# Performance work log

Hardware: AMD Instinct MI355X
Metric: run time of the kernel (lower is better)

## Reference

```python
import jax, jax.numpy as jnp
import numpy as np

B, I, C, H, QP, VP = 2, 1024, 16, 12, 4, 8
W_C = (2.0 / (9.0 * QP)) ** 0.5
W_L = (1.0 / 3.0) ** 0.5


def setup_inputs() -> dict:
    key = jax.random.key(0)
    ks = jax.random.split(key, 14)
    rn = lambda k, shape, s=1.0: (jax.random.normal(k, shape, dtype=jnp.float32) * s)
    return {
        "s": rn(ks[0], (B, I, C)),
        "z": rn(ks[1], (B, I, I, C)),
        "R": rn(ks[2], (B, I, 3, 3)),
        "t": rn(ks[3], (B, I, 3)),
        "Wq": rn(ks[4], (C, C * H), C ** -0.5),
        "Wk": rn(ks[5], (C, C * H), C ** -0.5),
        "Wv": rn(ks[6], (C, C * H), C ** -0.5),
        "Wb": rn(ks[7], (C, H), C ** -0.5),
        "Wqp": rn(ks[8], (C, 3 * QP * H), C ** -0.5),
        "Wkp": rn(ks[9], (C, 3 * QP * H), C ** -0.5),
        "Wvp": rn(ks[10], (C, 3 * VP * H), C ** -0.5),
        "gamma": rn(ks[11], (H,), 0.5),
        "Wout": rn(ks[12], (H * (2 * C + 4 * VP), C), (H * (2 * C + 4 * VP)) ** -0.5),
        "bout": rn(ks[13], (C,), 0.02),
    }


def _apply_rigid(R, t, p):
    # p: (B, i, n, 3); rigid transform per residue: R @ p + t
    return jnp.einsum("bixy,bipy->bipx", R, p) + t[:, :, None, :]


def reference(s, z, R, t, Wq, Wk, Wv, Wb, Wqp, Wkp, Wvp, gamma, Wout, bout):
    b_, i_, c = s.shape
    h, qp, vp = gamma.shape[0], Wqp.shape[1] // (3 * gamma.shape[0]), Wvp.shape[1] // (3 * gamma.shape[0])

    q = (s @ Wq).reshape(b_, i_, h, c)
    k = (s @ Wk).reshape(b_, i_, h, c)
    v = (s @ Wv).reshape(b_, i_, h, c)

    q_pts = _apply_rigid(R, t, (s @ Wqp).reshape(b_, i_, h * qp, 3)).reshape(b_, i_, h, qp, 3)
    k_pts = _apply_rigid(R, t, (s @ Wkp).reshape(b_, i_, h * qp, 3)).reshape(b_, i_, h, qp, 3)
    v_pts = _apply_rigid(R, t, (s @ Wvp).reshape(b_, i_, h * vp, 3)).reshape(b_, i_, h, vp, 3)

    bias = jnp.einsum("bijc,ch->bhij", z, Wb)
    a = jnp.einsum("bihc,bjhc->bhij", q, k) * (c ** -0.5) + bias

    # squared point distances summed over points, expanded to avoid (B,i,j,h,P,3) tensor
    q2 = jnp.sum(q_pts ** 2, axis=(-1, -2))          # (B,i,h)
    k2 = jnp.sum(k_pts ** 2, axis=(-1, -2))          # (B,j,h)
    qk = jnp.einsum("bihpx,bjhpx->bhij", q_pts, k_pts)
    d2 = q2.transpose(0, 2, 1)[..., None] + k2.transpose(0, 2, 1)[:, :, None, :] - 2.0 * qk  # (B,h,i,j)

    head_w = jax.nn.softplus(gamma)                  # (h,)
    a = a + d2 * (head_w[None, :, None, None] * W_C * -0.5)
    a = a * W_L
    a = jax.nn.softmax(a, axis=-2)  # NOTE: original code softmaxes over dim=-2 (the i axis)

    # NOTE: original einsum indexes v by i (not j); replicated faithfully
    o = jnp.einsum("bhij,bihc->bihc", a, v).reshape(b_, i_, h * c)

    o_pts = jnp.einsum("bhij,bjhpx->bihpx", a, v_pts)  # (B,i,h,vp,3)
    o_pts_norm = jnp.sqrt(jnp.maximum(jnp.sum(o_pts ** 2, axis=-1), 1e-12)).reshape(b_, i_, h * vp)
    o_pts_flat = o_pts.reshape(b_, i_, h * vp * 3)

    o_pair = jnp.einsum("bhij,bijc->bihc", a, z).reshape(b_, i_, h * c)

    cat = jnp.concatenate([o, o_pair, o_pts_flat, o_pts_norm], axis=-1)
    return cat @ Wout + bout
```

## Files before the change

kernel.cpp:

```cpp
#include <hip/hip_runtime.h>
#include <hip/hip_bf16.h>
#include <math.h>

#define B_ 2
#define I_ 1024
#define C_ 16
#define H_ 12
#define ICH 8

__device__ __constant__ float kW_C = 0.23570226039551584f;
#define W_Lc 0.5773502691896258f
#define LOG2E 1.4426950408889634f

typedef _Float16 hf;
typedef hf hf2 __attribute__((ext_vector_type(2)));
typedef hf hf4v __attribute__((ext_vector_type(4)));
typedef hf hf8v __attribute__((ext_vector_type(8)));
typedef float f32x4 __attribute__((ext_vector_type(4)));
typedef unsigned int u32;

template <typename T, typename F>
__device__ inline T bc(F f) { return __builtin_bit_cast(T, f); }

__device__ inline float fdot2f(u32 a, u32 b, float c) {
#if __has_builtin(__builtin_amdgcn_fdot2)
  return __builtin_amdgcn_fdot2(bc<hf2>(a), bc<hf2>(b), c, false);
#else
  hf2 x = bc<hf2>(a), y = bc<hf2>(b);
  return c + (float)x[0] * (float)y[0] + (float)x[1] * (float)y[1];
#endif
}

__device__ inline u32 pkrtz(float lo, float hi) {
#if __has_builtin(__builtin_amdgcn_cvt_pkrtz)
  return bc<u32>(__builtin_amdgcn_cvt_pkrtz(lo, hi));
#else
  hf2 t; t[0] = (hf)lo; t[1] = (hf)hi; return bc<u32>(t);
#endif
}

__device__ inline u32 permlo(u32 hiw, u32 low) {
#if __has_builtin(__builtin_amdgcn_perm)
  return __builtin_amdgcn_perm(hiw, low, 0x05040100u);
#else
  return (low & 0xffffu) | (hiw << 16);
#endif
}
__device__ inline u32 permhi(u32 hiw, u32 low) {
#if __has_builtin(__builtin_amdgcn_perm)
  return __builtin_amdgcn_perm(hiw, low, 0x07060302u);
#else
  return (low >> 16) | (hiw & 0xffff0000u);
#endif
}

#define QF16_OFF 0
#define QF16_SZ (B_*I_*196)
#define KF16_OFF (QF16_OFF + QF16_SZ)
#define KF16_SZ QF16_SZ
#define VPF_OFF (KF16_OFF + KF16_SZ)
#define VPF_SZ (B_*I_*144)
#define VV_OFF (VPF_OFF + VPF_SZ)
#define VV_SZ (B_*I_*192)
#define SM_OFF (VV_OFF + VV_SZ)
#define SM_SZ (B_*12*1024*2)
#define PM_OFF (SM_OFF + SM_SZ)
#define PM_SZ (B_*64*ICH*192*2)
#define LT_OFF (PM_OFF + PM_SZ)
#define LT_SZ (B_*H_*512*1024)
#define ACC2_OFF (LT_OFF + LT_SZ)

__global__ __launch_bounds__(192) void kA(const float* __restrict__ s, const float* __restrict__ R,
                 const float* __restrict__ t, const float* __restrict__ Wq,
                 const float* __restrict__ Wk, const float* __restrict__ Wv,
                 const float* __restrict__ Wqp, const float* __restrict__ Wkp,
                 const float* __restrict__ Wvp, const float* __restrict__ gam,
                 float* __restrict__ ws) {
  int blk = blockIdx.x;
  int b = blk >> 10, i = blk & 1023;
  int tid = threadIdx.x;
  __shared__ float sl[16], rl[9], tl[3], part[96];
  if (tid < 16) sl[tid] = s[(b*I_ + i)*C_ + tid];
  else if (tid < 25) rl[tid-16] = R[(size_t)(b*I_+i)*9 + (tid-16)];
  else if (tid < 28) tl[tid-25] = t[(size_t)(b*I_+i)*3 + (tid-25)];
  __syncthreads();
  hf* QF  = (hf*)(ws + QF16_OFF) + (size_t)(b*I_+i)*392;
  hf* KF  = (hf*)(ws + KF16_OFF) + (size_t)(b*I_+i)*392;
  ushort* VPP = (ushort*)(ws + VPF_OFF);
  float* vv = ws + VV_OFF + (size_t)(b*I_+i)*192;
  {
    int hc = tid; int h = hc >> 4, c = hc & 15;
    float aq = 0.f, ak = 0.f, av = 0.f;
    #pragma unroll
    for (int ci = 0; ci < 16; ci++) {
      float sv = sl[ci];
      aq += sv * Wq[ci*192 + hc];
      ak += sv * Wk[ci*192 + hc];
      av += sv * Wv[ci*192 + hc];
    }
    const float s_qk = 0.25f * W_Lc * LOG2E;
    QF[h*32 + c] = (hf)(aq * s_qk);
    KF[h*32 + c] = (hf)ak;
    vv[hc] = av;
  }
  {
    float raw[3], px[3];
    if (tid < 96) {
      bool isq = tid < 48;
      int n = isq ? tid : tid - 48;
      const float* W = isq ? Wqp : Wkp;
      #pragma unroll
      for (int x = 0; x < 3; x++) {
        float a2 = 0.f;
        #pragma unroll
        for (int ci = 0; ci < 16; ci++) a2 += sl[ci] * W[ci*144 + n*3 + x];
        raw[x] = a2;
      }
      #pragma unroll
      for (int x = 0; x < 3; x++)
        px[x] = rl[x*3]*raw[0] + rl[x*3+1]*raw[1] + rl[x*3+2]*raw[2] + tl[x];
      int h = n >> 2, p = n & 3;
      part[tid] = px[0]*px[0] + px[1]*px[1] + px[2]*px[2];
      if (isq) {
        float g = gam[h];
        float sp = log1pf(expf(g));
        float coef2 = -0.5f * kW_C * sp * W_Lc * LOG2E;
        #pragma unroll
        for (int x = 0; x < 3; x++) QF[h*32 + 16 + p*3 + x] = (hf)(px[x] * (-2.0f * coef2));
      } else {
        #pragma unroll
        for (int x = 0; x < 3; x++) KF[h*32 + 16 + p*3 + x] = (hf)px[x];
      }
    } else {
      int n = tid - 96;
      #pragma unroll
      for (int x = 0; x < 3; x++) {
        float a2 = 0.f;
        #pragma unroll
        for (int ci = 0; ci < 16; ci++) a2 += sl[ci] * Wvp[ci*288 + n*3 + x];
        raw[x] = a2;
      }
      #pragma unroll
      for (int x = 0; x < 3; x++)
        px[x] = rl[x*3]*raw[0] + rl[x*3+1]*raw[1] + rl[x*3+2]*raw[2] + tl[x];
      int h = n >> 3, p = n & 7;
      size_t base = ((size_t)(b*512 + (i >> 1))*12 + h)*48 + (i & 1);
      #pragma unroll
      for (int x = 0; x < 3; x++) VPP[base + (p*3 + x)*2] = bc<ushort>((hf)px[x]);
    }
  }
  __syncthreads();
  if (tid < 24) {
    int h = tid % 12; bool isq = tid < 12;
    float g = gam[h];
    float sp = log1pf(expf(g));
    float coef2 = -0.5f * kW_C * sp * W_Lc * LOG2E;
    float s2 = 0.f;
    int base = isq ? h*4 : 48 + h*4;
    #pragma unroll
    for (int p = 0; p < 4; p++) s2 += part[base + p];
    if (isq) {
      QF[h*32 + 28] = (hf)(coef2 * s2);
      QF[h*32 + 29] = (hf)1.0f;
      QF[h*32 + 30] = (hf)0.0f;
      QF[h*32 + 31] = (hf)0.0f;
    } else {
      KF[h*32 + 28] = (hf)1.0f;
      KF[h*32 + 29] = (hf)(coef2 * s2);
      KF[h*32 + 30] = (hf)0.0f;
      KF[h*32 + 31] = (hf)0.0f;
    }
  }
}

__global__ __launch_bounds__(256,4) void kB(const float* __restrict__ z,
                 const float* __restrict__ Wb, float* __restrict__ ws) {
  int blk = blockIdx.x;
  int ic = blk & (ICH-1); int jt = (blk >> 3) & 63; int b = blk >> 9;
  int tid = threadIdx.x;
  int w = tid >> 6, lane = tid & 63;
  int ln15 = lane & 15, l16 = lane >> 4;
  int j0 = jt*16;
  __shared__ ushort qlds[16*392];
  __shared__ u32 lqk[12*16*18];
  __shared__ ushort lbias[16*208];
  __shared__ u32 llog[96*17];
  hf8v kf[3];
  #pragma unroll
  for (int q = 0; q < 3; q++) {
    int h = w*3 + q;
    const ushort* src = (const ushort*)(ws + KF16_OFF) + ((size_t)(b*I_ + j0 + ln15)*392 + h*32 + l16*8);
    kf[q] = *(const hf8v*)src;
  }
  hf4v wbf;
  #pragma unroll
  for (int e = 0; e < 4; e++) {
    int c = l16*4 + e;
    float v = (ln15 < 12) ? Wb[c*12 + ln15] * (W_Lc*LOG2E) : 0.f;
    wbf[e] = (hf)v;
  }
  u32* LTu_w = (u32*)(ws + LT_OFF);
  float m = -1e30f, S = 0.f;
  for (int t = 0; t < 8; ++t) {
    int i0 = ic*128 + t*16;
    __syncthreads();
    {
      const uint4* qsrc = (const uint4*)((const hf*)(ws + QF16_OFF) + (size_t)(b*I_+i0)*392);
      uint4* qdst = (uint4*)qlds;
      for (int idx = tid; idx < 784; idx += 256) qdst[idx] = qsrc[idx];
    }
    __syncthreads();
    #pragma unroll
    for (int q = 0; q < 3; q++) {
      int h = w*3 + q;
      hf8v a = *(const hf8v*)&qlds[ln15*392 + h*32 + l16*8];
      f32x4 c = {0.f, 0.f, 0.f, 0.f};
      c = __builtin_amdgcn_mfma_f32_16x16x32_f16(a, kf[q], c, 0, 0, 0);
      u32* dst = &lqk[(h*16 + ln15)*18 + l16*4];
      *(uint2*)dst     = make_uint2(bc<u32>(c[0]), bc<u32>(c[1]));
      *(uint2*)(dst+2) = make_uint2(bc<u32>(c[2]), bc<u32>(c[3]));
    }
    #pragma unroll
    for (int r = 0; r < 4; r++) {
      int ii = w*4 + r;
      float4 zv = *(const float4*)(z + ((size_t)(b*I_ + i0 + ii)*I_ + j0 + ln15)*16 + l16*4);
      uint2 ap = make_uint2(pkrtz(zv.x, zv.y), pkrtz(zv.z, zv.w));
      hf4v a = bc<hf4v>(ap);
      f32x4 cb = {0.f, 0.f, 0.f, 0.f};
      cb = __builtin_amdgcn_mfma_f32_16x16x16f16(a, wbf, cb, 0, 0, 0);
      if (ln15 < 12) {
        #pragma unroll
        for (int reg = 0; reg < 4; reg++) {
          int jj = l16*4 + reg;
          lbias[ii*208 + jj*13 + ln15] = bc<ushort>((hf)cb[reg]);
        }
      }
    }
    __syncthreads();
    if (tid < 192) {
      int h = tid >> 4, jl = tid & 15;
      const u32* qk = &lqk[(h*16 + jl)*18];
      float l[16];
      #pragma unroll
      for (int i = 0; i < 16; i++) l[i] = bc<float>(qk[i]);
      #pragma unroll
      for (int i = 0; i < 16; i++) l[i] += (float)bc<hf>(lbias[i*208 + jl*13 + h]);
      u32 lw[8];
      #pragma unroll
      for (int p = 0; p < 8; p++) lw[p] = pkrtz(l[2*p], l[2*p+1]);
      float lr[16];
      #pragma unroll
      for (int p = 0; p < 8; p++) { hf2 lh = bc<hf2>(lw[p]); lr[2*p] = (float)lh[0]; lr[2*p+1] = (float)lh[1]; }
      float m8[8];
      #pragma unroll
      for (int p = 0; p < 8; p++) m8[p] = fmaxf(lr[2*p], lr[2*p+1]);
      float mt = fmaxf(fmaxf(fmaxf(m8[0],m8[1]), fmaxf(m8[2],m8[3])),
                       fmaxf(fmaxf(m8[4],m8[5]), fmaxf(m8[6],m8[7])));
      float e[16];
      #pragma unroll
      for (int p = 0; p < 16; p++) e[p] = __builtin_amdgcn_exp2f(lr[p] - mt);
      float st = ((e[0]+e[1])+(e[2]+e[3])) + ((e[4]+e[5])+(e[6]+e[7]))
               + ((e[8]+e[9])+(e[10]+e[11])) + ((e[12]+e[13])+(e[14]+e[15]));
      float mn = fmaxf(m, mt);
      S = S * __builtin_amdgcn_exp2f(m - mn) + st * __builtin_amdgcn_exp2f(mt - mn);
      m = mn;
      #pragma unroll
      for (int p = 0; p < 8; p++) {
        u32 pw = (u32)__shfl_xor((int)lw[p], 1);
        u32 ex = (jl & 1) ? permhi(lw[p], pw) : permlo(pw, lw[p]);
        llog[(h*8 + (jl>>1))*17 + 2*p + (jl&1)] = ex;
      }
    }
    __syncthreads();
    if (tid < 192) {
      int row = tid >> 1, iseg = (tid & 1) << 3;
      const u32* lr2 = &llog[row*17 + iseg];
      u32 o0=lr2[0],o1=lr2[1],o2=lr2[2],o3=lr2[3],o4=lr2[4],o5=lr2[5],o6=lr2[6],o7=lr2[7];
      int hh = row >> 3, jpg2 = row & 7;
      u32* dst = LTu_w + ((size_t)(b*12+hh)*512 + jt*8 + jpg2)*1024 + i0 + iseg;
      *(uint4*)dst = make_uint4(o0,o1,o2,o3);
      *(uint4*)(dst+4) = make_uint4(o4,o5,o6,o7);
    }
  }
  if (tid < 192) {
    float2* pm = (float2*)(ws + PM_OFF);
    pm[((size_t)(b*64+jt)*ICH + ic)*192 + tid] = make_float2(m, S);
  }
}

__global__ __launch_bounds__(192) void kB2(float* __restrict__ ws) {
  int blk = blockIdx.x; int jt = blk & 63, b = blk >> 6;
  int tid = threadIdx.x; int h = tid >> 4, jl = tid & 15;
  const float2* pm = (const float2*)(ws + PM_OFF) + (size_t)(b*64+jt)*ICH*192 + tid;
  float m = -1e30f, S = 0.f;
  #pragma unroll
  for (int ic = 0; ic < ICH; ic++) {
    float2 p = pm[ic*192];
    float mn = fmaxf(m, p.x);
    S = S * __builtin_amdgcn_exp2f(m - mn) + p.y * __builtin_amdgcn_exp2f(p.x - mn);
    m = mn;
  }
  int j = jt*16 + jl;
  float* sm = ws + SM_OFF + ((size_t)((b*12+h)*1024) + j)*2;
  sm[0] = m;
  sm[1] = 1.0f / S;
}

__global__ __launch_bounds__(192,6) void kC(const float* __restrict__ z,
                 float* __restrict__ ws, int jsh) {
  int blk = blockIdx.x;
  int jch = 1 << jsh;
  int jc = blk & (jch-1); int it = (blk >> jsh) & 63; int b = blk >> (jsh+6);
  int tid = threadIdx.x; int h = tid >> 4, il = tid & 15;
  int i = it*16 + il;
  __shared__ u32 llds[96*18];
  __shared__ u32 zplds[16*132];
  float opts[24], opair[16], rsum = 0.f;
  #pragma unroll
  for (int n = 0; n < 24; n++) opts[n] = 0.f;
  #pragma unroll
  for (int c = 0; c < 16; c++) opair[c] = 0.f;
  const u32* LTu = (const u32*)(ws + LT_OFF);
  const float* SM = ws + SM_OFF + (size_t)((b*12+h)*1024)*2;
  const ushort* VPP = (const ushort*)(ws + VPF_OFF);
  int chunk = I_ >> jsh;
  int nt = chunk >> 4;
  int hh = tid >> 4, rr = tid & 15, sjp = rr >> 1, sq = rr & 1;
  for (int t = 0; t < nt; ++t) {
    int j0 = jc*chunk + t*16;
    int jpg0 = j0 >> 1;
    __syncthreads();
    {
      const u32* src = LTu + ((size_t)(b*12+hh)*512 + jpg0 + sjp)*1024 + it*16 + sq*8;
      uint4 a = *(const uint4*)src;
      uint4 c4 = *(const uint4*)(src + 4);
      u32* drow = llds + (hh*8 + sjp)*18 + sq*8;
      *(uint2*)(drow + 0) = make_uint2(a.x, a.y);
      *(uint2*)(drow + 2) = make_uint2(a.z, a.w);
      *(uint2*)(drow + 4) = make_uint2(c4.x, c4.y);
      *(uint2*)(drow + 6) = make_uint2(c4.z, c4.w);
    }
    for (int idx = tid; idx < 512; idx += 192) {
      int r = idx >> 5, jp = (idx >> 2) & 7, c4 = idx & 3;
      const float* zb = z + ((size_t)(b*I_ + it*16 + r)*I_ + j0 + 2*jp)*16 + c4*4;
      float4 a = *(const float4*)zb;
      float4 d = *(const float4*)(zb + 16);
      uint4 o = make_uint4(pkrtz(a.x, d.x), pkrtz(a.y, d.y), pkrtz(a.z, d.z), pkrtz(a.w, d.w));
      *(uint4*)&zplds[r*132 + jp*16 + c4*4] = o;
    }
    __syncthreads();
    #pragma unroll 1
    for (int jp = 0; jp < 8; ++jp) {
      u32 lp = llds[(h*8 + jp)*18 + il];
      float4 st = *(const float4*)(SM + (size_t)(j0 + 2*jp)*2);
      const uint4* vp4 = (const uint4*)(VPP + ((size_t)(b*512 + jpg0 + jp)*12 + h)*48);
      uint4 va = vp4[0], vb = vp4[1], vc = vp4[2];
      uint4 vd = vp4[3], ve = vp4[4], vf = vp4[5];
      hf2 lh = bc<hf2>(lp);
      float w0 = __builtin_amdgcn_exp2f((float)lh[0] - st.x) * st.y;
      float w1 = __builtin_amdgcn_exp2f((float)lh[1] - st.z) * st.w;
      rsum += w0 + w1;
      u32 w2 = pkrtz(w0, w1);
      const u32* zr = &zplds[il*132 + jp*16];
      uint4 p0 = *(const uint4*)(zr + 0), p1 = *(const uint4*)(zr + 4);
      uint4 p2 = *(const uint4*)(zr + 8), p3 = *(const uint4*)(zr + 12);
      opair[0]  = fdot2f(w2, p0.x, opair[0]);
      opair[1]  = fdot2f(w2, p0.y, opair[1]);
      opair[2]  = fdot2f(w2, p0.z, opair[2]);
      opair[3]  = fdot2f(w2, p0.w, opair[3]);
      opair[4]  = fdot2f(w2, p1.x, opair[4]);
      opair[5]  = fdot2f(w2, p1.y, opair[5]);
      opair[6]  = fdot2f(w2, p1.z, opair[6]);
      opair[7]  = fdot2f(w2, p1.w, opair[7]);
      opair[8]  = fdot2f(w2, p2.x, opair[8]);
      opair[9]  = fdot2f(w2, p2.y, opair[9]);
      opair[10] = fdot2f(w2, p2.z, opair[10]);
      opair[11] = fdot2f(w2, p2.w, opair[11]);
      opair[12] = fdot2f(w2, p3.x, opair[12]);
      opair[13] = fdot2f(w2, p3.y, opair[13]);
      opair[14] = fdot2f(w2, p3.z, opair[14]);
      opair[15] = fdot2f(w2, p3.w, opair[15]);
      opts[0]  = fdot2f(w2, va.x, opts[0]);
      opts[1]  = fdot2f(w2, va.y, opts[1]);
      opts[2]  = fdot2f(w2, va.z, opts[2]);
      opts[3]  = fdot2f(w2, va.w, opts[3]);
      opts[4]  = fdot2f(w2, vb.x, opts[4]);
      opts[5]  = fdot2f(w2, vb.y, opts[5]);
      opts[6]  = fdot2f(w2, vb.z, opts[6]);
      opts[7]  = fdot2f(w2, vb.w, opts[7]);
      opts[8]  = fdot2f(w2, vc.x, opts[8]);
      opts[9]  = fdot2f(w2, vc.y, opts[9]);
      opts[10] = fdot2f(w2, vc.z, opts[10]);
      opts[11] = fdot2f(w2, vc.w, opts[11]);
      opts[12] = fdot2f(w2, vd.x, opts[12]);
      opts[13] = fdot2f(w2, vd.y, opts[13]);
      opts[14] = fdot2f(w2, vd.z, opts[14]);
      opts[15] = fdot2f(w2, vd.w, opts[15]);
      opts[16] = fdot2f(w2, ve.x, opts[16]);
      opts[17] = fdot2f(w2, ve.y, opts[17]);
      opts[18] = fdot2f(w2, ve.z, opts[18]);
      opts[19] = fdot2f(w2, ve.w, opts[19]);
      opts[20] = fdot2f(w2, vf.x, opts[20]);
      opts[21] = fdot2f(w2, vf.y, opts[21]);
      opts[22] = fdot2f(w2, vf.z, opts[22]);
      opts[23] = fdot2f(w2, vf.w, opts[23]);
    }
  }
  ushort* ab = (ushort*)(ws + ACC2_OFF) + ((size_t)(b*I_+i)*jch + jc)*512;
  #pragma unroll
  for (int n = 0; n < 24; n++) ab[h*24 + n] = bc<ushort>((hf)opts[n]);
  #pragma unroll
  for (int c = 0; c < 16; c++) ab[288 + h*16 + c] = bc<ushort>((hf)opair[c]);
  ab[480 + h] = bc<ushort>((hf)rsum);
}

__global__ __launch_bounds__(256) void kD(const float* __restrict__ Wout, const float* __restrict__ bout,
                 const float* __restrict__ ws, float* __restrict__ out, int jsh) {
  int jch = 1 << jsh;
  int blk = blockIdx.x;
  int b = blk >> 8; int i0 = (blk & 255) << 2;
  int tid = threadIdx.x;
  __shared__ float accs[4*512];
  __shared__ float cat[4*776];
  __shared__ float red[256];
  const ushort* ACC2us = (const ushort*)(ws + ACC2_OFF);
  for (int idx = tid; idx < 4*512; idx += 256) {
    int r = idx >> 9, f = idx & 511;
    const ushort* src = ACC2us + (size_t)(b*I_+i0+r)*jch*512 + f;
    float ssum = 0.f;
    for (int jc = 0; jc < jch; jc++) ssum += (float)bc<hf>(src[jc*512]);
    accs[idx] = ssum;
  }
  __syncthreads();
  const float* vv = ws + VV_OFF;
  for (int idx = tid; idx < 4*768; idx += 256) {
    int r = idx / 768, f = idx - r*768;
    int i = i0 + r;
    const float* ab = accs + r*512;
    float val;
    if (f < 192) {
      int h = f >> 4, c = f & 15;
      val = vv[(size_t)(b*I_+i)*192 + h*16 + c] * ab[480 + h];
    } else if (f < 384) {
      val = ab[288 + (f - 192)];
    } else if (f < 672) {
      val = ab[f - 384];
    } else {
      int g = f - 672; int base = (g >> 3)*24 + (g & 7)*3;
      float x0 = ab[base], x1 = ab[base+1], x2 = ab[base+2];
      val = sqrtf(fmaxf(x0*x0 + x1*x1 + x2*x2, 1e-12f));
    }
    cat[r*776 + f] = val;
  }
  __syncthreads();
  {
    int r = tid >> 6, c = (tid >> 2) & 15, sseg = tid & 3;
    const float* cr = cat + r*776;
    float a = 0.f;
    for (int f = sseg*192; f < sseg*192 + 192; f++) a += cr[f] * Wout[f*16 + c];
    red[tid] = a;
  }
  __syncthreads();
  if ((tid & 3) == 0) {
    int r = tid >> 6, c = (tid >> 2) & 15;
    float sum = bout[c] + red[tid] + red[tid+1] + red[tid+2] + red[tid+3];
    out[((size_t)(b*I_) + i0 + r)*16 + c] = sum;
  }
}

extern "C" void kernel_launch(void* const* d_in, const int* in_sizes, int n_in,
                              void* d_out, int out_size, void* d_ws, size_t ws_size,
                              hipStream_t stream) {
  const float* s    = (const float*)d_in[0];
  const float* z    = (const float*)d_in[1];
  const float* R    = (const float*)d_in[2];
  const float* t    = (const float*)d_in[3];
  const float* Wq   = (const float*)d_in[4];
  const float* Wk   = (const float*)d_in[5];
  const float* Wv   = (const float*)d_in[6];
  const float* Wb   = (const float*)d_in[7];
  const float* Wqp  = (const float*)d_in[8];
  const float* Wkp  = (const float*)d_in[9];
  const float* Wvp  = (const float*)d_in[10];
  const float* gam  = (const float*)d_in[11];
  const float* Wout = (const float*)d_in[12];
  const float* bout = (const float*)d_in[13];
  float* out = (float*)d_out;
  float* ws = (float*)d_ws;

  int jsh = 4;
  while (jsh > 0) {
    size_t need = ((size_t)ACC2_OFF + (size_t)B_*I_*(1u<<jsh)*256) * 4u;
    if (need <= ws_size) break;
    jsh--;
  }

  hipLaunchKernelGGL(kA, dim3(B_*I_), dim3(192), 0, stream,
                     s, R, t, Wq, Wk, Wv, Wqp, Wkp, Wvp, gam, ws);
  hipLaunchKernelGGL(kB, dim3(B_*64*ICH), dim3(256), 0, stream, z, Wb, ws);
  hipLaunchKernelGGL(kB2, dim3(B_*64), dim3(192), 0, stream, ws);
  hipLaunchKernelGGL(kC, dim3(B_*64*(1<<jsh)), dim3(192), 0, stream, z, ws, jsh);
  hipLaunchKernelGGL(kD, dim3(B_*256), dim3(256), 0, stream, Wout, bout, ws, out, jsh);
}
```

Measured before the change: 172.9 us.

## Prefetch z tiles into registers and drop LDS staging of logits in kB

The bias kernel now loads the next i-tile of z into registers while computing the current tile, so the large z global reads overlap with the MFMA and softmax work. Bias values are packed two-per-word and stored with a single vector write instead of scattered 16-bit LDS stores. The llog LDS transpose, with its extra barrier, is replaced by a second lane shuffle, so each thread writes its logit block straight to global memory. The loop-top barrier is also removed, since the existing barriers still order the shared-buffer reuse. In exchange, register pressure rises from the four prefetched float4 values and the extra shuffle arrays, which could hurt occupancy under launch_bounds(256,4).

```diff
diff --git a/kernel.cpp b/kernel.cpp
--- a/kernel.cpp
+++ b/kernel.cpp
@@ -183,8 +183,7 @@
   int j0 = jt*16;
   __shared__ ushort qlds[16*392];
   __shared__ u32 lqk[12*16*18];
-  __shared__ ushort lbias[16*208];
-  __shared__ u32 llog[96*17];
+  __shared__ u32 lbias32[16*112];
   hf8v kf[3];
   #pragma unroll
   for (int q = 0; q < 3; q++) {
@@ -201,9 +200,16 @@
   }
   u32* LTu_w = (u32*)(ws + LT_OFF);
   float m = -1e30f, S = 0.f;
+  float4 zb0, zb1, zb2, zb3;
+  {
+    const float* zbase = z + ((size_t)(b*I_ + ic*128 + w*4)*I_ + j0 + ln15)*16 + l16*4;
+    zb0 = *(const float4*)(zbase);
+    zb1 = *(const float4*)(zbase + (size_t)I_*16);
+    zb2 = *(const float4*)(zbase + (size_t)I_*32);
+    zb3 = *(const float4*)(zbase + (size_t)I_*48);
+  }
   for (int t = 0; t < 8; ++t) {
     int i0 = ic*128 + t*16;
-    __syncthreads();
     {
       const uint4* qsrc = (const uint4*)((const hf*)(ws + QF16_OFF) + (size_t)(b*I_+i0)*392);
       uint4* qdst = (uint4*)qlds;
@@ -222,19 +228,24 @@
     }
     #pragma unroll
     for (int r = 0; r < 4; r++) {
+      float4 zv = (r == 0) ? zb0 : (r == 1) ? zb1 : (r == 2) ? zb2 : zb3;
       int ii = w*4 + r;
-      float4 zv = *(const float4*)(z + ((size_t)(b*I_ + i0 + ii)*I_ + j0 + ln15)*16 + l16*4);
       uint2 ap = make_uint2(pkrtz(zv.x, zv.y), pkrtz(zv.z, zv.w));
       hf4v a = bc<hf4v>(ap);
       f32x4 cb = {0.f, 0.f, 0.f, 0.f};
       cb = __builtin_amdgcn_mfma_f32_16x16x16f16(a, wbf, cb, 0, 0, 0);
       if (ln15 < 12) {
-        #pragma unroll
-        for (int reg = 0; reg < 4; reg++) {
-          int jj = l16*4 + reg;
-          lbias[ii*208 + jj*13 + ln15] = bc<ushort>((hf)cb[reg]);
-        }
+        u32 b01 = pkrtz(cb[0], cb[1]);
+        u32 b23 = pkrtz(cb[2], cb[3]);
+        *(uint2*)&lbias32[ii*112 + ln15*9 + l16*2] = make_uint2(b01, b23);
       }
+    }
+    if (t < 7) {
+      const float* zbase = z + ((size_t)(b*I_ + ic*128 + (t+1)*16 + w*4)*I_ + j0 + ln15)*16 + l16*4;
+      zb0 = *(const float4*)(zbase);
+      zb1 = *(const float4*)(zbase + (size_t)I_*16);
+      zb2 = *(const float4*)(zbase + (size_t)I_*32);
+      zb3 = *(const float4*)(zbase + (size_t)I_*48);
     }
     __syncthreads();
     if (tid < 192) {
@@ -242,9 +253,11 @@
       const u32* qk = &lqk[(h*16 + jl)*18];
       float l[16];
       #pragma unroll
-      for (int i = 0; i < 16; i++) l[i] = bc<float>(qk[i]);
-      #pragma unroll
-      for (int i = 0; i < 16; i++) l[i] += (float)bc<hf>(lbias[i*208 + jl*13 + h]);
+      for (int i = 0; i < 16; i++) {
+        u32 bb = lbias32[i*112 + h*9 + (jl >> 1)];
+        ushort bu = (jl & 1) ? (ushort)(bb >> 16) : (ushort)(bb & 0xffffu);
+        l[i] = bc<float>(qk[i]) + (float)bc<hf>(bu);
+      }
       u32 lw[8];
       #pragma unroll
       for (int p = 0; p < 8; p++) lw[p] = pkrtz(l[2*p], l[2*p+1]);
@@ -264,22 +277,27 @@
       float mn = fmaxf(m, mt);
       S = S * __builtin_amdgcn_exp2f(m - mn) + st * __builtin_amdgcn_exp2f(mt - mn);
       m = mn;
+      u32 ex[8];
       #pragma unroll
       for (int p = 0; p < 8; p++) {
         u32 pw = (u32)__shfl_xor((int)lw[p], 1);
-        u32 ex = (jl & 1) ? permhi(lw[p], pw) : permlo(pw, lw[p]);
-        llog[(h*8 + (jl>>1))*17 + 2*p + (jl&1)] = ex;
+        ex[p] = (jl & 1) ? permhi(lw[p], pw) : permlo(pw, lw[p]);
       }
-    }
-    __syncthreads();
-    if (tid < 192) {
-      int row = tid >> 1, iseg = (tid & 1) << 3;
-      const u32* lr2 = &llog[row*17 + iseg];
-      u32 o0=lr2[0],o1=lr2[1],o2=lr2[2],o3=lr2[3],o4=lr2[4],o5=lr2[5],o6=lr2[6],o7=lr2[7];
-      int hh = row >> 3, jpg2 = row & 7;
-      u32* dst = LTu_w + ((size_t)(b*12+hh)*512 + jt*8 + jpg2)*1024 + i0 + iseg;
-      *(uint4*)dst = make_uint4(o0,o1,o2,o3);
-      *(uint4*)(dst+4) = make_uint4(o4,o5,o6,o7);
+      u32 sw[8];
+      #pragma unroll
+      for (int p = 0; p < 8; p++) sw[p] = (u32)__shfl_xor((int)ex[p], 1);
+      int par = jl & 1;
+      u32 o0 = par ? sw[4] : ex[0];
+      u32 o1 = par ? ex[4] : sw[0];
+      u32 o2 = par ? sw[5] : ex[1];
+      u32 o3 = par ? ex[5] : sw[1];
+      u32 o4 = par ? sw[6] : ex[2];
+      u32 o5 = par ? ex[6] : sw[2];
+      u32 o6 = par ? sw[7] : ex[3];
+      u32 o7 = par ? ex[7] : sw[3];
+      u32* dst = LTu_w + ((size_t)(b*12+h)*512 + jt*8 + (jl>>1))*1024 + i0 + par*8;
+      *(uint4*)dst     = make_uint4(o0, o1, o2, o3);
+      *(uint4*)(dst+4) = make_uint4(o4, o5, o6, o7);
     }
   }
   if (tid < 192) {
```

Measured after the change: 172.7 us. Within noise of the previous version (-0.1%).

## Restructure logit kernel to per-wave independent i-chunks without block barriers

Applied to the files above, without the earlier changes.

The logit/bias kernel now assigns each wave its own 32-row i-chunk and processes all 12 heads per wave. It computes QK MFMA with fragments loaded directly from global memory and does the softmax max/sum reduction with cross-lane shuffles in registers. This removes the shared-memory staging of Q, the four __syncthreads per iteration and the transpose buffer. Partial softmax stats grow from 8 to 32 chunks per j-tile, so the merge kernel does more work. Q/K fragments are re-read from global/L2 by every wave.

```diff
diff --git a/kernel.cpp b/kernel.cpp
--- a/kernel.cpp
+++ b/kernel.cpp
@@ -6,7 +6,6 @@
 #define I_ 1024
 #define C_ 16
 #define H_ 12
-#define ICH 8
 
 __device__ __constant__ float kW_C = 0.23570226039551584f;
 #define W_Lc 0.5773502691896258f
@@ -65,7 +64,7 @@
 #define SM_OFF (VV_OFF + VV_SZ)
 #define SM_SZ (B_*12*1024*2)
 #define PM_OFF (SM_OFF + SM_SZ)
-#define PM_SZ (B_*64*ICH*192*2)
+#define PM_SZ (B_*64*32*192*2)
 #define LT_OFF (PM_OFF + PM_SZ)
 #define LT_SZ (B_*H_*512*1024)
 #define ACC2_OFF (LT_OFF + LT_SZ)
@@ -176,22 +175,16 @@
 __global__ __launch_bounds__(256,4) void kB(const float* __restrict__ z,
                  const float* __restrict__ Wb, float* __restrict__ ws) {
   int blk = blockIdx.x;
-  int ic = blk & (ICH-1); int jt = (blk >> 3) & 63; int b = blk >> 9;
+  int icb = blk & 7; int jt = (blk >> 3) & 63; int b = blk >> 9;
   int tid = threadIdx.x;
   int w = tid >> 6, lane = tid & 63;
   int ln15 = lane & 15, l16 = lane >> 4;
   int j0 = jt*16;
-  __shared__ ushort qlds[16*392];
-  __shared__ u32 lqk[12*16*18];
-  __shared__ ushort lbias[16*208];
-  __shared__ u32 llog[96*17];
-  hf8v kf[3];
-  #pragma unroll
-  for (int q = 0; q < 3; q++) {
-    int h = w*3 + q;
-    const ushort* src = (const ushort*)(ws + KF16_OFF) + ((size_t)(b*I_ + j0 + ln15)*392 + h*32 + l16*8);
-    kf[q] = *(const hf8v*)src;
-  }
+  int icw = icb*4 + w;
+  __shared__ u32 lb[4*16*113];
+  int wbase = w*(16*113);
+  const ushort* QFu = (const ushort*)(ws + QF16_OFF);
+  const ushort* KFu = (const ushort*)(ws + KF16_OFF);
   hf4v wbf;
   #pragma unroll
   for (int e = 0; e < 4; e++) {
@@ -200,101 +193,73 @@
     wbf[e] = (hf)v;
   }
   u32* LTu_w = (u32*)(ws + LT_OFF);
-  float m = -1e30f, S = 0.f;
-  for (int t = 0; t < 8; ++t) {
-    int i0 = ic*128 + t*16;
-    __syncthreads();
-    {
-      const uint4* qsrc = (const uint4*)((const hf*)(ws + QF16_OFF) + (size_t)(b*I_+i0)*392);
-      uint4* qdst = (uint4*)qlds;
-      for (int idx = tid; idx < 784; idx += 256) qdst[idx] = qsrc[idx];
-    }
-    __syncthreads();
-    #pragma unroll
-    for (int q = 0; q < 3; q++) {
-      int h = w*3 + q;
-      hf8v a = *(const hf8v*)&qlds[ln15*392 + h*32 + l16*8];
-      f32x4 c = {0.f, 0.f, 0.f, 0.f};
-      c = __builtin_amdgcn_mfma_f32_16x16x32_f16(a, kf[q], c, 0, 0, 0);
-      u32* dst = &lqk[(h*16 + ln15)*18 + l16*4];
-      *(uint2*)dst     = make_uint2(bc<u32>(c[0]), bc<u32>(c[1]));
-      *(uint2*)(dst+2) = make_uint2(bc<u32>(c[2]), bc<u32>(c[3]));
-    }
-    #pragma unroll
-    for (int r = 0; r < 4; r++) {
-      int ii = w*4 + r;
+  float m[12], S[12];
+  #pragma unroll
+  for (int h = 0; h < 12; h++) { m[h] = -1e30f; S[h] = 0.f; }
+  for (int tt = 0; tt < 2; ++tt) {
+    int i0 = icw*32 + tt*16;
+    #pragma unroll 4
+    for (int ii = 0; ii < 16; ++ii) {
       float4 zv = *(const float4*)(z + ((size_t)(b*I_ + i0 + ii)*I_ + j0 + ln15)*16 + l16*4);
       uint2 ap = make_uint2(pkrtz(zv.x, zv.y), pkrtz(zv.z, zv.w));
       hf4v a = bc<hf4v>(ap);
       f32x4 cb = {0.f, 0.f, 0.f, 0.f};
       cb = __builtin_amdgcn_mfma_f32_16x16x16f16(a, wbf, cb, 0, 0, 0);
       if (ln15 < 12) {
-        #pragma unroll
-        for (int reg = 0; reg < 4; reg++) {
-          int jj = l16*4 + reg;
-          lbias[ii*208 + jj*13 + ln15] = bc<ushort>((hf)cb[reg]);
-        }
+        lb[wbase + ii*113 + ln15*9 + l16*2]     = pkrtz(cb[0], cb[1]);
+        lb[wbase + ii*113 + ln15*9 + l16*2 + 1] = pkrtz(cb[2], cb[3]);
       }
     }
-    __syncthreads();
-    if (tid < 192) {
-      int h = tid >> 4, jl = tid & 15;
-      const u32* qk = &lqk[(h*16 + jl)*18];
-      float l[16];
-      #pragma unroll
-      for (int i = 0; i < 16; i++) l[i] = bc<float>(qk[i]);
-      #pragma unroll
-      for (int i = 0; i < 16; i++) l[i] += (float)bc<hf>(lbias[i*208 + jl*13 + h]);
-      u32 lw[8];
-      #pragma unroll
-      for (int p = 0; p < 8; p++) lw[p] = pkrtz(l[2*p], l[2*p+1]);
-      float lr[16];
-      #pragma unroll
-      for (int p = 0; p < 8; p++) { hf2 lh = bc<hf2>(lw[p]); lr[2*p] = (float)lh[0]; lr[2*p+1] = (float)lh[1]; }
-      float m8[8];
-      #pragma unroll
-      for (int p = 0; p < 8; p++) m8[p] = fmaxf(lr[2*p], lr[2*p+1]);
-      float mt = fmaxf(fmaxf(fmaxf(m8[0],m8[1]), fmaxf(m8[2],m8[3])),
-                       fmaxf(fmaxf(m8[4],m8[5]), fmaxf(m8[6],m8[7])));
-      float e[16];
-      #pragma unroll
-      for (int p = 0; p < 16; p++) e[p] = __builtin_amdgcn_exp2f(lr[p] - mt);
-      float st = ((e[0]+e[1])+(e[2]+e[3])) + ((e[4]+e[5])+(e[6]+e[7]))
-               + ((e[8]+e[9])+(e[10]+e[11])) + ((e[12]+e[13])+(e[14]+e[15]));
-      float mn = fmaxf(m, mt);
-      S = S * __builtin_amdgcn_exp2f(m - mn) + st * __builtin_amdgcn_exp2f(mt - mn);
-      m = mn;
-      #pragma unroll
-      for (int p = 0; p < 8; p++) {
-        u32 pw = (u32)__shfl_xor((int)lw[p], 1);
-        u32 ex = (jl & 1) ? permhi(lw[p], pw) : permlo(pw, lw[p]);
-        llog[(h*8 + (jl>>1))*17 + 2*p + (jl&1)] = ex;
+    #pragma unroll
+    for (int h = 0; h < 12; ++h) {
+      hf8v aq = *(const hf8v*)&QFu[(size_t)(b*I_ + i0 + ln15)*392 + h*32 + l16*8];
+      hf8v bk = *(const hf8v*)&KFu[(size_t)(b*I_ + j0 + ln15)*392 + h*32 + l16*8];
+      f32x4 c = {0.f, 0.f, 0.f, 0.f};
+      c = __builtin_amdgcn_mfma_f32_16x16x32_f16(aq, bk, c, 0, 0, 0);
+      int ib = wbase + (l16*4)*113 + h*9 + (ln15 >> 1);
+      int par = (ln15 & 1) << 4;
+      float l0 = c[0] + (float)bc<hf>((ushort)(lb[ib]       >> par));
+      float l1 = c[1] + (float)bc<hf>((ushort)(lb[ib + 113] >> par));
+      float l2 = c[2] + (float)bc<hf>((ushort)(lb[ib + 226] >> par));
+      float l3 = c[3] + (float)bc<hf>((ushort)(lb[ib + 339] >> par));
+      hf h0 = (hf)l0, h1 = (hf)l1, h2 = (hf)l2, h3 = (hf)l3;
+      float r0 = (float)h0, r1 = (float)h1, r2 = (float)h2, r3 = (float)h3;
+      float mx = fmaxf(fmaxf(r0, r1), fmaxf(r2, r3));
+      mx = fmaxf(mx, __shfl_xor(mx, 16));
+      mx = fmaxf(mx, __shfl_xor(mx, 32));
+      float es = __builtin_amdgcn_exp2f(r0 - mx) + __builtin_amdgcn_exp2f(r1 - mx)
+               + __builtin_amdgcn_exp2f(r2 - mx) + __builtin_amdgcn_exp2f(r3 - mx);
+      es += __shfl_xor(es, 16);
+      es += __shfl_xor(es, 32);
+      float mn = fmaxf(m[h], mx);
+      S[h] = S[h] * __builtin_amdgcn_exp2f(m[h] - mn) + es * __builtin_amdgcn_exp2f(mx - mn);
+      m[h] = mn;
+      u32 me01 = (u32)bc<ushort>(h0) | ((u32)bc<ushort>(h1) << 16);
+      u32 me23 = (u32)bc<ushort>(h2) | ((u32)bc<ushort>(h3) << 16);
+      u32 p01 = (u32)__shfl_xor((int)me01, 1);
+      u32 p23 = (u32)__shfl_xor((int)me23, 1);
+      if ((ln15 & 1) == 0) {
+        u32 w0 = permlo(p01, me01), w1 = permhi(p01, me01);
+        u32 w2 = permlo(p23, me23), w3 = permhi(p23, me23);
+        u32* dst = LTu_w + ((size_t)(b*12 + h)*512 + jt*8 + (ln15 >> 1))*1024 + i0 + l16*4;
+        *(uint4*)dst = make_uint4(w0, w1, w2, w3);
       }
     }
-    __syncthreads();
-    if (tid < 192) {
-      int row = tid >> 1, iseg = (tid & 1) << 3;
-      const u32* lr2 = &llog[row*17 + iseg];
-      u32 o0=lr2[0],o1=lr2[1],o2=lr2[2],o3=lr2[3],o4=lr2[4],o5=lr2[5],o6=lr2[6],o7=lr2[7];
-      int hh = row >> 3, jpg2 = row & 7;
-      u32* dst = LTu_w + ((size_t)(b*12+hh)*512 + jt*8 + jpg2)*1024 + i0 + iseg;
-      *(uint4*)dst = make_uint4(o0,o1,o2,o3);
-      *(uint4*)(dst+4) = make_uint4(o4,o5,o6,o7);
-    }
-  }
-  if (tid < 192) {
-    float2* pm = (float2*)(ws + PM_OFF);
-    pm[((size_t)(b*64+jt)*ICH + ic)*192 + tid] = make_float2(m, S);
+  }
+  if (l16 == 0) {
+    float2* pm = (float2*)(ws + PM_OFF) + ((size_t)((b*64 + jt)*32 + icw))*192;
+    #pragma unroll
+    for (int h = 0; h < 12; ++h) pm[h*16 + ln15] = make_float2(m[h], S[h]);
   }
 }
 
 __global__ __launch_bounds__(192) void kB2(float* __restrict__ ws) {
   int blk = blockIdx.x; int jt = blk & 63, b = blk >> 6;
   int tid = threadIdx.x; int h = tid >> 4, jl = tid & 15;
-  const float2* pm = (const float2*)(ws + PM_OFF) + (size_t)(b*64+jt)*ICH*192 + tid;
+  const float2* pm = (const float2*)(ws + PM_OFF) + (size_t)(b*64+jt)*32*192 + tid;
   float m = -1e30f, S = 0.f;
   #pragma unroll
-  for (int ic = 0; ic < ICH; ic++) {
+  for (int ic = 0; ic < 32; ic++) {
     float2 p = pm[ic*192];
     float mn = fmaxf(m, p.x);
     S = S * __builtin_amdgcn_exp2f(m - mn) + p.y * __builtin_amdgcn_exp2f(p.x - mn);
@@ -497,7 +462,7 @@
 
   hipLaunchKernelGGL(kA, dim3(B_*I_), dim3(192), 0, stream,
                      s, R, t, Wq, Wk, Wv, Wqp, Wkp, Wvp, gam, ws);
-  hipLaunchKernelGGL(kB, dim3(B_*64*ICH), dim3(256), 0, stream, z, Wb, ws);
+  hipLaunchKernelGGL(kB, dim3(B_*64*8), dim3(256), 0, stream, z, Wb, ws);
   hipLaunchKernelGGL(kB2, dim3(B_*64), dim3(192), 0, stream, ws);
   hipLaunchKernelGGL(kC, dim3(B_*64*(1<<jsh)), dim3(192), 0, stream, z, ws, jsh);
   hipLaunchKernelGGL(kD, dim3(B_*256), dim3(256), 0, stream, Wout, bout, ws, out, jsh);
```

After: 177.2 us. 2.5% more time.
